# Performance work log

Hardware: AMD Instinct MI355X
Metric: run time of the kernel (lower is better)

## Reference

```python
import jax, jax.numpy as jnp
import numpy as np

N_INPUT = 24
N_HIDDEN = 128
N_OUTPUT = 1
BATCH = 4096
T = 336

def setup_inputs() -> dict:
    key = jax.random.key(0)
    ks = jax.random.split(key, 11)
    s = lambda fan: 1.0 / np.sqrt(fan)
    return {
        "x": jax.random.normal(ks[0], (BATCH, T, 2 * N_INPUT), dtype=jnp.float32),
        "Wih": jax.random.normal(ks[1], (3 * N_HIDDEN, N_INPUT), dtype=jnp.float32) * s(N_HIDDEN),
        "Whh": jax.random.normal(ks[2], (3 * N_HIDDEN, N_HIDDEN), dtype=jnp.float32) * s(N_HIDDEN),
        "bih": jax.random.normal(ks[3], (3 * N_HIDDEN,), dtype=jnp.float32) * s(N_HIDDEN),
        "bhh": jax.random.normal(ks[4], (3 * N_HIDDEN,), dtype=jnp.float32) * s(N_HIDDEN),
        "h2o_W": jax.random.normal(ks[5], (N_OUTPUT, N_HIDDEN), dtype=jnp.float32) * s(N_HIDDEN),
        "h2o_b": jax.random.normal(ks[6], (N_OUTPUT,), dtype=jnp.float32) * s(N_HIDDEN),
        "W1_W": jax.random.normal(ks[7], (N_INPUT, N_HIDDEN), dtype=jnp.float32) * s(N_HIDDEN),
        "W1_b": jax.random.normal(ks[8], (N_INPUT,), dtype=jnp.float32) * s(N_HIDDEN),
        "W2_W": jax.random.normal(ks[9], (N_INPUT, N_INPUT), dtype=jnp.float32) * s(N_INPUT),
        "W2_b": jax.random.normal(ks[10], (N_INPUT,), dtype=jnp.float32) * s(N_INPUT),
    }

def _gru_a_forward(x, Wih, Whh, bih, bhh, h2o_W, h2o_b, W1_W, W1_b, W2_W, W2_b):
    B = x.shape[0]
    H = Whh.shape[1]
    I = Wih.shape[1]

    def step(carry, xt):
        hidden, a1, a2 = carry
        h1 = xt[:, :I]          # [B, I]
        h2 = xt[:, I:]          # [B, I]
        c = a1 * h1 + a2 * h2   # attention-gated input
        # torch.nn.GRUCell math
        gx = c @ Wih.T + bih          # [B, 3H]
        gh = hidden @ Whh.T + bhh     # [B, 3H]
        r = jax.nn.sigmoid(gx[:, :H] + gh[:, :H])
        z = jax.nn.sigmoid(gx[:, H:2 * H] + gh[:, H:2 * H])
        n = jnp.tanh(gx[:, 2 * H:] + r * gh[:, 2 * H:])
        hidden = (1.0 - z) * n + z * hidden
        out = jnp.tanh(hidden @ h2o_W.T + h2o_b)   # [B, 1]
        w1h = hidden @ W1_W.T + W1_b               # [B, I]
        e1 = jnp.exp(jnp.tanh(w1h + h1 @ W2_W.T + W2_b))
        e2 = jnp.exp(jnp.tanh(w1h + h2 @ W2_W.T + W2_b))
        denom = e1 + e2
        return (hidden, e1 / denom, e2 / denom), out

    init = (jnp.zeros((B, H), x.dtype),
            jnp.ones((B, I), x.dtype),
            jnp.zeros((B, I), x.dtype))
    xs = jnp.swapaxes(x, 0, 1)                     # [T, B, 2I]
    _, outs = jax.lax.scan(step, init, xs)          # [T, B, 1]
    return jnp.swapaxes(outs, 0, 1).squeeze(2)      # [B, T]

def reference(x, Wih, Whh, bih, bhh, h2o_W, h2o_b, W1_W, W1_b, W2_W, W2_b):
    return _gru_a_forward(x, Wih, Whh, bih, bhh, h2o_W, h2o_b, W1_W, W1_b, W2_W, W2_b)
```

## Files before the change

### kernel.cpp

```cpp
#include <hip/hip_runtime.h>

#define TSTEPS 336
#define NI 24
#define NH 128
#define RW 16
#define NTHREADS 512
#define NWG 256

typedef __attribute__((ext_vector_type(8))) short bf16x8;
typedef __attribute__((ext_vector_type(4))) float f32x4;
typedef unsigned short u16;
typedef unsigned int u32;

struct __align__(16) Smem {
    u16 hhi[4][72][8];
    u16 chi[64][8], clo[64][8];
    u16 x1hi[64][8], x2hi[64][8];
    float xt[2][16][52];
    u16 w1f[2][4][64][8];
    u16 w2f[2][64][8];
    u16 h2of[4][64][8];
};
static_assert(sizeof(Smem) <= 32768, "LDS overflow for 2 WG/CU");

__device__ __forceinline__ u16 f2bf(float f) {
    u32 u = __float_as_uint(f);
    return (u16)((u + 0x7FFFu + ((u >> 16) & 1u)) >> 16);
}
__device__ __forceinline__ float bf2f(u16 h) { return __uint_as_float(((u32)h) << 16); }
__device__ __forceinline__ float frcp(float x) { return __builtin_amdgcn_rcpf(x); }
__device__ __forceinline__ float fex2(float x) { return __builtin_amdgcn_exp2f(x); }
__device__ __forceinline__ float sigm(float x) { return frcp(1.0f + fex2(-1.4426950408889634f * x)); }
__device__ __forceinline__ float tanhf_(float x) { return 1.0f - 2.0f * frcp(1.0f + fex2(2.8853900817779268f * x)); }
__device__ __forceinline__ float fexp(float x) { return fex2(1.4426950408889634f * x); }

__device__ __forceinline__ bf16x8 ldfrag(const float* __restrict__ p) {
    float4 a = *(const float4*)p;
    float4 b = *(const float4*)(p + 4);
    union { u32 u[4]; bf16x8 v; } r;
    r.u[0] = (u32)f2bf(a.x) | ((u32)f2bf(a.y) << 16);
    r.u[1] = (u32)f2bf(a.z) | ((u32)f2bf(a.w) << 16);
    r.u[2] = (u32)f2bf(b.x) | ((u32)f2bf(b.y) << 16);
    r.u[3] = (u32)f2bf(b.z) | ((u32)f2bf(b.w) << 16);
    return r.v;
}

__device__ __forceinline__ void bar() {
    asm volatile("s_waitcnt lgkmcnt(0)" ::: "memory");
    __builtin_amdgcn_s_barrier();
    asm volatile("" ::: "memory");
}

#define MFMA(A, B, C) __builtin_amdgcn_mfma_f32_16x16x32_bf16((A), (B), (C), 0, 0, 0)

__global__ __launch_bounds__(NTHREADS, 2) void gru_persist(
    const float* __restrict__ x, const float* __restrict__ wih, const float* __restrict__ whh,
    const float* __restrict__ bih, const float* __restrict__ bhh,
    const float* __restrict__ h2ow, const float* __restrict__ h2ob_p,
    const float* __restrict__ w1w, const float* __restrict__ w1b_p,
    const float* __restrict__ w2w, const float* __restrict__ w2b_p,
    float* __restrict__ out)
{
    __shared__ Smem S;
    const int tid = threadIdx.x;
    const int l = tid & 63;
    const int w = tid >> 6;
    const int g = l >> 4;
    const int cl = l & 15;
    const int b0 = blockIdx.x * RW;

    for (int i = tid; i < (int)(sizeof(Smem) / 4); i += NTHREADS) ((u32*)&S)[i] = 0u;
    bar();

    for (int idx = tid; idx < NI * NH; idx += NTHREADS) {
        int c = idx >> 7, k = idx & 127;
        S.w1f[c >> 4][k >> 5][(c & 15) + ((k >> 3) & 3) * 16][k & 7] = f2bf(w1w[idx]);
    }
    for (int idx = tid; idx < NI * NI; idx += NTHREADS) {
        int c = idx / NI, k = idx - c * NI;
        S.w2f[c >> 4][(c & 15) + (k >> 3) * 16][k & 7] = f2bf(w2w[idx]);
    }
    for (int k = tid; k < NH; k += NTHREADS)
        S.h2of[k >> 5][((k >> 3) & 3) * 16][k & 7] = f2bf(h2ow[k]);
    if (tid < 192) {
        int row = tid / 12, c4 = (tid % 12) * 4;
        *(float4*)&S.xt[0][row][c4] = *(const float4*)(x + ((size_t)(b0 + row) * TSTEPS) * 48 + c4);
        *(float4*)&S.xt[1][row][c4] = *(const float4*)(x + ((size_t)(b0 + row) * TSTEPS + 1) * 48 + c4);
    }

    const bf16x8 zf = {0, 0, 0, 0, 0, 0, 0, 0};
    bf16x8 wihR[3], whhR[3][4];
#pragma unroll
    for (int s = 0; s < 3; ++s) {
        const int tw = w + 8 * s;
        wihR[s] = (l < 48) ? ldfrag(wih + (16 * tw + cl) * NI + 8 * g) : zf;
#pragma unroll
        for (int kt = 0; kt < 4; ++kt)
            whhR[s][kt] = ldfrag(whh + (16 * tw + cl) * NH + 32 * kt + 8 * g);
    }

    const int u = 16 * w + cl;
    const float bR  = bih[u] + bhh[u];
    const float bZ  = bih[128 + u] + bhh[128 + u];
    const float bxN = bih[256 + u];
    const float bhN = bhh[256 + u];
    const float w1b_c = (w == 0) ? w1b_p[cl] : ((w == 1 && cl < 8) ? w1b_p[16 + cl] : 0.0f);
    const float w2b_c = (w == 0) ? w2b_p[cl] : ((w == 1 && cl < 8) ? w2b_p[16 + cl] : 0.0f);
    const float h2ob = h2ob_p[0];

    const int ktH = w >> 1;
    const int cc = (2 * w + (cl >> 3)) & 3;
    const int hsB0 = 4 * g + 16 * cc + (g >> 1) + 2 * cc;
    const int eH = cl & 7;
    const int hsl = l + ((l >> 3) & 1) + 2 * (l >> 4);
    const int jC = 16 * w + cl;
    const int cSlotB = ((jC >> 3) & 3) * 16;
    const int cEl = jC & 7;
    const bool isC = (w == 0) || (w == 1 && cl < 8);

    float h_reg[4] = {0.f, 0.f, 0.f, 0.f};

    bar();

    if (tid < 384) {
        int rr = tid & 15, j = tid >> 4;
        float xh1 = S.xt[0][rr][j];
        float xh2 = S.xt[0][rr][24 + j];
        int lane = rr + (j >> 3) * 16, el = j & 7;
        u16 hi = f2bf(xh1);
        S.chi[lane][el] = hi;  S.clo[lane][el] = f2bf(xh1 - bf2f(hi));
        S.x1hi[lane][el] = hi;
        S.x2hi[lane][el] = f2bf(xh2);
    }
    f32x4 gR = {bR, bR, bR, bR};
    f32x4 gZ = {bZ, bZ, bZ, bZ};
    f32x4 gN = {bhN, bhN, bhN, bhN};
    __syncthreads();

    for (int t = 0; t < TSTEPS; ++t) {
        const int nxt = (t + 1) & 1;
        float4 xf;
        const bool isLd = (tid >= 320) && (t + 2 < TSTEPS);
        if (isLd) {
            int e = tid - 320, row = e / 12, c4 = (e % 12) * 4;
            xf = *(const float4*)(x + ((size_t)(b0 + row) * TSTEPS + (t + 2)) * 48 + c4);
        }
        f32x4 aN = {bxN, bxN, bxN, bxN};
        f32x4 s1a, s2a;
        {
            bf16x8 cH = *(const bf16x8*)&S.chi[l][0];
            bf16x8 cL = *(const bf16x8*)&S.clo[l][0];
            gR = MFMA(cH, wihR[0], gR);  gR = MFMA(cL, wihR[0], gR);
            gZ = MFMA(cH, wihR[1], gZ);  gZ = MFMA(cL, wihR[1], gZ);
            aN = MFMA(cH, wihR[2], aN);  aN = MFMA(cL, wihR[2], aN);
        }
        if (w < 2) {
            bf16x8 w2frag = *(const bf16x8*)&S.w2f[w][l][0];
            bf16x8 x1f = *(const bf16x8*)&S.x1hi[l][0];
            bf16x8 x2f = *(const bf16x8*)&S.x2hi[l][0];
            s1a = (f32x4){w2b_c, w2b_c, w2b_c, w2b_c};
            s2a = (f32x4){w2b_c, w2b_c, w2b_c, w2b_c};
            s1a = MFMA(x1f, w2frag, s1a);
            s2a = MFMA(x2f, w2frag, s2a);
        }
#pragma unroll
        for (int i = 0; i < 4; ++i) {
            float r = sigm(gR[i]);
            float z = sigm(gZ[i]);
            float n = tanhf_(aN[i] + r * gN[i]);
            float hv = (1.0f - z) * n + z * h_reg[i];
            h_reg[i] = hv;
            S.hhi[ktH][hsB0 + i][eH] = f2bf(hv);
        }
        bar();
        gR = (f32x4){bR, bR, bR, bR};
        gZ = (f32x4){bZ, bZ, bZ, bZ};
        gN = (f32x4){bhN, bhN, bhN, bhN};
        f32x4 whacc = {w1b_c, w1b_c, w1b_c, w1b_c};
#pragma unroll
        for (int kt = 0; kt < 4; ++kt) {
            bf16x8 hH = *(const bf16x8*)&S.hhi[kt][hsl][0];
            gR = MFMA(hH, whhR[0][kt], gR);
            gZ = MFMA(hH, whhR[1][kt], gZ);
            gN = MFMA(hH, whhR[2][kt], gN);
            if (w < 3) {
                bf16x8 hA = (w < 2) ? *(const bf16x8*)&S.w1f[w][kt][l][0]
                                    : *(const bf16x8*)&S.h2of[kt][l][0];
                whacc = MFMA(hH, hA, whacc);
            }
        }
        if (w == 2) {
            if (cl == 0) {
#pragma unroll
                for (int i = 0; i < 4; ++i)
                    out[(size_t)(b0 + 4 * g + i) * TSTEPS + t] = tanhf_(whacc[i] + h2ob);
            }
        } else if (isC) {
#pragma unroll
            for (int i = 0; i < 4; ++i) {
                float v = whacc[i];
                float e1 = fexp(tanhf_(v + s1a[i]));
                float e2 = fexp(tanhf_(v + s2a[i]));
                float inv = frcp(e1 + e2);
                int row = 4 * g + i;
                float xh1 = S.xt[nxt][row][jC];
                float xh2 = S.xt[nxt][row][24 + jC];
                float cv = (e1 * inv) * xh1 + (e2 * inv) * xh2;
                u16 hi = f2bf(cv);
                S.chi[row + cSlotB][cEl] = hi;
                S.clo[row + cSlotB][cEl] = f2bf(cv - bf2f(hi));
            }
        }
        if (tid >= 128) {
            int e = tid - 128, rr = e & 15, j = e >> 4;
            float v1 = S.xt[nxt][rr][j];
            float v2 = S.xt[nxt][rr][24 + j];
            int slot = rr + (j >> 3) * 16, el = j & 7;
            S.x1hi[slot][el] = f2bf(v1);
            S.x2hi[slot][el] = f2bf(v2);
        }
        if (isLd) {
            int e = tid - 320, row = e / 12, c4 = (e % 12) * 4;
            *(float4*)&S.xt[t & 1][row][c4] = xf;
        }
        bar();
    }
}

extern "C" void kernel_launch(void* const* d_in, const int* in_sizes, int n_in,
                              void* d_out, int out_size, void* d_ws, size_t ws_size,
                              hipStream_t stream) {
    const float* x    = (const float*)d_in[0];
    const float* wih  = (const float*)d_in[1];
    const float* whh  = (const float*)d_in[2];
    const float* bih  = (const float*)d_in[3];
    const float* bhh  = (const float*)d_in[4];
    const float* h2ow = (const float*)d_in[5];
    const float* h2ob = (const float*)d_in[6];
    const float* w1w  = (const float*)d_in[7];
    const float* w1b  = (const float*)d_in[8];
    const float* w2w  = (const float*)d_in[9];
    const float* w2b  = (const float*)d_in[10];
    float* out = (float*)d_out;

    gru_persist<<<NWG, NTHREADS, 0, stream>>>(x, wih, whh, bih, bhh,
                                              h2ow, h2ob, w1w, w1b, w2w, w2b, out);
}
```

Before: 460.9 us.

## Interleave two independent batch groups per workgroup to overlap GRU phases

Each workgroup now handles 32 batch rows as two independent 16-row groups, with half the grid size. Each step runs one group's input/gate phase alongside the other group's hidden-matmul/attention phase, staggered by half a step, so both halves of the recurrence are filled between barriers. The x staging buffer becomes triple-buffered per group so the next-step attention data stays valid while prefetches land. The cost is doubled LDS and register state, fewer workgroups (down to one per CU) and longer per-step dependency chains.

```diff
diff --git a/kernel.cpp b/kernel.cpp
--- a/kernel.cpp
+++ b/kernel.cpp
@@ -3,9 +3,9 @@
 #define TSTEPS 336
 #define NI 24
 #define NH 128
-#define RW 16
+#define RW 32
 #define NTHREADS 512
-#define NWG 256
+#define NWG 128
 
 typedef __attribute__((ext_vector_type(8))) short bf16x8;
 typedef __attribute__((ext_vector_type(4))) float f32x4;
@@ -13,15 +13,15 @@
 typedef unsigned int u32;
 
 struct __align__(16) Smem {
-    u16 hhi[4][72][8];
-    u16 chi[64][8], clo[64][8];
-    u16 x1hi[64][8], x2hi[64][8];
-    float xt[2][16][52];
+    u16 hhi[2][4][72][8];
+    u16 chi[2][64][8], clo[2][64][8];
+    u16 x1hi[2][64][8], x2hi[2][64][8];
+    float xt[2][3][16][52];
     u16 w1f[2][4][64][8];
     u16 w2f[2][64][8];
     u16 h2of[4][64][8];
 };
-static_assert(sizeof(Smem) <= 32768, "LDS overflow for 2 WG/CU");
+static_assert(sizeof(Smem) <= 65536, "LDS overflow");
 
 __device__ __forceinline__ u16 f2bf(float f) {
     u32 u = __float_as_uint(f);
@@ -84,8 +84,14 @@
         S.h2of[k >> 5][((k >> 3) & 3) * 16][k & 7] = f2bf(h2ow[k]);
     if (tid < 192) {
         int row = tid / 12, c4 = (tid % 12) * 4;
-        *(float4*)&S.xt[0][row][c4] = *(const float4*)(x + ((size_t)(b0 + row) * TSTEPS) * 48 + c4);
-        *(float4*)&S.xt[1][row][c4] = *(const float4*)(x + ((size_t)(b0 + row) * TSTEPS + 1) * 48 + c4);
+        const float* base = x + (size_t)(b0 + row) * TSTEPS * 48 + c4;
+        *(float4*)&S.xt[0][0][row][c4] = *(const float4*)base;
+        *(float4*)&S.xt[0][1][row][c4] = *(const float4*)(base + 48);
+    } else if (tid >= 320) {
+        int e = tid - 320, row = e / 12, c4 = (e % 12) * 4;
+        const float* base = x + (size_t)(b0 + 16 + row) * TSTEPS * 48 + c4;
+        *(float4*)&S.xt[1][0][row][c4] = *(const float4*)base;
+        *(float4*)&S.xt[1][1][row][c4] = *(const float4*)(base + 48);
     }
 
     const bf16x8 zf = {0, 0, 0, 0, 0, 0, 0, 0};
@@ -118,71 +124,63 @@
     const int cEl = jC & 7;
     const bool isC = (w == 0) || (w == 1 && cl < 8);
 
-    float h_reg[4] = {0.f, 0.f, 0.f, 0.f};
-
+    float h0[4] = {0.f, 0.f, 0.f, 0.f};
+    float h1v[4] = {0.f, 0.f, 0.f, 0.f};
     bar();
 
     if (tid < 384) {
         int rr = tid & 15, j = tid >> 4;
-        float xh1 = S.xt[0][rr][j];
-        float xh2 = S.xt[0][rr][24 + j];
         int lane = rr + (j >> 3) * 16, el = j & 7;
-        u16 hi = f2bf(xh1);
-        S.chi[lane][el] = hi;  S.clo[lane][el] = f2bf(xh1 - bf2f(hi));
-        S.x1hi[lane][el] = hi;
-        S.x2hi[lane][el] = f2bf(xh2);
-    }
-    f32x4 gR = {bR, bR, bR, bR};
-    f32x4 gZ = {bZ, bZ, bZ, bZ};
-    f32x4 gN = {bhN, bhN, bhN, bhN};
+#pragma unroll
+        for (int q = 0; q < 2; ++q) {
+            float xh1 = S.xt[q][0][rr][j];
+            u16 hi = f2bf(xh1);
+            S.chi[q][lane][el] = hi;
+            S.clo[q][lane][el] = f2bf(xh1 - bf2f(hi));
+        }
+    }
+    f32x4 gR0 = {bR, bR, bR, bR}, gZ0 = {bZ, bZ, bZ, bZ}, gN0 = {bhN, bhN, bhN, bhN};
+    f32x4 gR1 = gR0, gZ1 = gZ0, gN1 = gN0;
     __syncthreads();
 
-    for (int t = 0; t < TSTEPS; ++t) {
-        const int nxt = (t + 1) & 1;
-        float4 xf;
-        const bool isLd = (tid >= 320) && (t + 2 < TSTEPS);
-        if (isLd) {
-            int e = tid - 320, row = e / 12, c4 = (e % 12) * 4;
-            xf = *(const float4*)(x + ((size_t)(b0 + row) * TSTEPS + (t + 2)) * 48 + c4);
-        }
+    auto do_p1 = [&](int q, f32x4& gRq, f32x4& gZq, f32x4& gNq, float* hregq) {
         f32x4 aN = {bxN, bxN, bxN, bxN};
+        bf16x8 cH = *(const bf16x8*)&S.chi[q][l][0];
+        bf16x8 cL = *(const bf16x8*)&S.clo[q][l][0];
+        gRq = MFMA(cH, wihR[0], gRq);  gRq = MFMA(cL, wihR[0], gRq);
+        gZq = MFMA(cH, wihR[1], gZq);  gZq = MFMA(cL, wihR[1], gZq);
+        aN  = MFMA(cH, wihR[2], aN);   aN  = MFMA(cL, wihR[2], aN);
+#pragma unroll
+        for (int i = 0; i < 4; ++i) {
+            float r = sigm(gRq[i]);
+            float z = sigm(gZq[i]);
+            float n = tanhf_(aN[i] + r * gNq[i]);
+            float hv = (1.0f - z) * n + z * hregq[i];
+            hregq[i] = hv;
+            S.hhi[q][ktH][hsB0 + i][eH] = f2bf(hv);
+        }
+    };
+    auto do_p2 = [&](int q, f32x4& gRq, f32x4& gZq, f32x4& gNq, int t_, int mnext) {
         f32x4 s1a, s2a;
-        {
-            bf16x8 cH = *(const bf16x8*)&S.chi[l][0];
-            bf16x8 cL = *(const bf16x8*)&S.clo[l][0];
-            gR = MFMA(cH, wihR[0], gR);  gR = MFMA(cL, wihR[0], gR);
-            gZ = MFMA(cH, wihR[1], gZ);  gZ = MFMA(cL, wihR[1], gZ);
-            aN = MFMA(cH, wihR[2], aN);  aN = MFMA(cL, wihR[2], aN);
-        }
         if (w < 2) {
             bf16x8 w2frag = *(const bf16x8*)&S.w2f[w][l][0];
-            bf16x8 x1f = *(const bf16x8*)&S.x1hi[l][0];
-            bf16x8 x2f = *(const bf16x8*)&S.x2hi[l][0];
+            bf16x8 x1f = *(const bf16x8*)&S.x1hi[q][l][0];
+            bf16x8 x2f = *(const bf16x8*)&S.x2hi[q][l][0];
             s1a = (f32x4){w2b_c, w2b_c, w2b_c, w2b_c};
             s2a = (f32x4){w2b_c, w2b_c, w2b_c, w2b_c};
             s1a = MFMA(x1f, w2frag, s1a);
             s2a = MFMA(x2f, w2frag, s2a);
         }
-#pragma unroll
-        for (int i = 0; i < 4; ++i) {
-            float r = sigm(gR[i]);
-            float z = sigm(gZ[i]);
-            float n = tanhf_(aN[i] + r * gN[i]);
-            float hv = (1.0f - z) * n + z * h_reg[i];
-            h_reg[i] = hv;
-            S.hhi[ktH][hsB0 + i][eH] = f2bf(hv);
-        }
-        bar();
-        gR = (f32x4){bR, bR, bR, bR};
-        gZ = (f32x4){bZ, bZ, bZ, bZ};
-        gN = (f32x4){bhN, bhN, bhN, bhN};
+        gRq = (f32x4){bR, bR, bR, bR};
+        gZq = (f32x4){bZ, bZ, bZ, bZ};
+        gNq = (f32x4){bhN, bhN, bhN, bhN};
         f32x4 whacc = {w1b_c, w1b_c, w1b_c, w1b_c};
 #pragma unroll
         for (int kt = 0; kt < 4; ++kt) {
-            bf16x8 hH = *(const bf16x8*)&S.hhi[kt][hsl][0];
-            gR = MFMA(hH, whhR[0][kt], gR);
-            gZ = MFMA(hH, whhR[1][kt], gZ);
-            gN = MFMA(hH, whhR[2][kt], gN);
+            bf16x8 hH = *(const bf16x8*)&S.hhi[q][kt][hsl][0];
+            gRq = MFMA(hH, whhR[0][kt], gRq);
+            gZq = MFMA(hH, whhR[1][kt], gZq);
+            gNq = MFMA(hH, whhR[2][kt], gNq);
             if (w < 3) {
                 bf16x8 hA = (w < 2) ? *(const bf16x8*)&S.w1f[w][kt][l][0]
                                     : *(const bf16x8*)&S.h2of[kt][l][0];
@@ -193,7 +191,7 @@
             if (cl == 0) {
 #pragma unroll
                 for (int i = 0; i < 4; ++i)
-                    out[(size_t)(b0 + 4 * g + i) * TSTEPS + t] = tanhf_(whacc[i] + h2ob);
+                    out[(size_t)(b0 + 16 * q + 4 * g + i) * TSTEPS + t_] = tanhf_(whacc[i] + h2ob);
             }
         } else if (isC) {
 #pragma unroll
@@ -203,28 +201,61 @@
                 float e2 = fexp(tanhf_(v + s2a[i]));
                 float inv = frcp(e1 + e2);
                 int row = 4 * g + i;
-                float xh1 = S.xt[nxt][row][jC];
-                float xh2 = S.xt[nxt][row][24 + jC];
+                float xh1 = S.xt[q][mnext][row][jC];
+                float xh2 = S.xt[q][mnext][row][24 + jC];
                 float cv = (e1 * inv) * xh1 + (e2 * inv) * xh2;
                 u16 hi = f2bf(cv);
-                S.chi[row + cSlotB][cEl] = hi;
-                S.clo[row + cSlotB][cEl] = f2bf(cv - bf2f(hi));
+                S.chi[q][row + cSlotB][cEl] = hi;
+                S.clo[q][row + cSlotB][cEl] = f2bf(cv - bf2f(hi));
             }
         }
+    };
+    auto rebuild = [&](int q, int mbuf) {
         if (tid >= 128) {
             int e = tid - 128, rr = e & 15, j = e >> 4;
-            float v1 = S.xt[nxt][rr][j];
-            float v2 = S.xt[nxt][rr][24 + j];
+            float v1 = S.xt[q][mbuf][rr][j];
+            float v2 = S.xt[q][mbuf][rr][24 + j];
             int slot = rr + (j >> 3) * 16, el = j & 7;
-            S.x1hi[slot][el] = f2bf(v1);
-            S.x2hi[slot][el] = f2bf(v2);
-        }
-        if (isLd) {
+            S.x1hi[q][slot][el] = f2bf(v1);
+            S.x2hi[q][slot][el] = f2bf(v2);
+        }
+    };
+
+    int m0 = 0;
+    for (int t = 0; t < TSTEPS; ++t) {
+        const int m1 = (m0 == 2) ? 0 : m0 + 1;
+        const int m2 = (m1 == 2) ? 0 : m1 + 1;
+        float4 xa;
+        const bool lda = (tid < 192) && (t + 2 < TSTEPS);
+        if (lda) {
+            int row = tid / 12, c4 = (tid % 12) * 4;
+            xa = *(const float4*)(x + ((size_t)(b0 + row) * TSTEPS + (t + 2)) * 48 + c4);
+        }
+        do_p1(0, gR0, gZ0, gN0, h0);
+        if (t >= 1) do_p2(1, gR1, gZ1, gN1, t - 1, m0);
+        rebuild(0, m0);
+        if (lda) {
+            int row = tid / 12, c4 = (tid % 12) * 4;
+            *(float4*)&S.xt[0][m2][row][c4] = xa;
+        }
+        bar();
+        float4 xb;
+        const bool ldb = (tid >= 320) && (t + 2 < TSTEPS);
+        if (ldb) {
             int e = tid - 320, row = e / 12, c4 = (e % 12) * 4;
-            *(float4*)&S.xt[t & 1][row][c4] = xf;
+            xb = *(const float4*)(x + ((size_t)(b0 + 16 + row) * TSTEPS + (t + 2)) * 48 + c4);
+        }
+        do_p2(0, gR0, gZ0, gN0, t, m1);
+        do_p1(1, gR1, gZ1, gN1, h1v);
+        rebuild(1, m0);
+        if (ldb) {
+            int e = tid - 320, row = e / 12, c4 = (e % 12) * 4;
+            *(float4*)&S.xt[1][m2][row][c4] = xb;
         }
         bar();
-    }
+        m0 = m1;
+    }
+    do_p2(1, gR1, gZ1, gN1, TSTEPS - 1, m0);
 }
 
 extern "C" void kernel_launch(void* const* d_in, const int* in_sizes, int n_in,
```

Measured after the change: 796.4 us. 72.8% more time.
